# Kernel optimization log

Hardware: AMD Instinct MI355X
Metric: run time of the kernel (lower is better)

The kernel has to match this reference:

```python
import jax, jax.numpy as jnp
import numpy as np

NUM_GROUPS = 32
EPS = 1e-5


def group_norm(x, scale, bias):
    # x: [b, c, h, w]
    b, c, h, w = x.shape
    xg = x.reshape(b, NUM_GROUPS, c // NUM_GROUPS, h, w)
    mean = jnp.mean(xg, axis=(2, 3, 4), keepdims=True)
    var = jnp.var(xg, axis=(2, 3, 4), keepdims=True)
    xg = (xg - mean) * jax.lax.rsqrt(var + EPS)
    xn = xg.reshape(b, c, h, w)
    return xn * scale[None, :, None, None] + bias[None, :, None, None]


def conv1x1(x, w, b):
    # x: [b, c_in, h, w], w: [c_out, c_in], b: [c_out]
    return jnp.einsum('bchw,dc->bdhw', x, w) + b[None, :, None, None]


def setup_inputs() -> dict:
    key = jax.random.key(0)
    ks = jax.random.split(key, 11)
    B, C, H, W = 16, 512, 32, 32
    s = 1.0 / np.sqrt(C)
    inp = {
        'x': jax.random.normal(ks[0], (B, C, H, W), jnp.float32),
        'gn_scale': jnp.ones((C,), jnp.float32),
        'gn_bias': jnp.zeros((C,), jnp.float32),
        'wq': jax.random.normal(ks[1], (C, C), jnp.float32) * s,
        'bq': jnp.zeros((C,), jnp.float32),
        'wk': jax.random.normal(ks[2], (C, C), jnp.float32) * s,
        'bk': jnp.zeros((C,), jnp.float32),
        'wv': jax.random.normal(ks[3], (C, C), jnp.float32) * s,
        'bv': jnp.zeros((C,), jnp.float32),
        'wp': jax.random.normal(ks[4], (C, C), jnp.float32) * s,
        'bp': jnp.zeros((C,), jnp.float32),
    }
    return inp


def reference(x, gn_scale, gn_bias, wq, bq, wk, bk, wv, bv, wp, bp):
    b, c, h, w = x.shape
    xn = group_norm(x, gn_scale, gn_bias)
    q = conv1x1(xn, wq, bq).reshape(b, c, h * w)  # [b, c, n]
    k = conv1x1(xn, wk, bk).reshape(b, c, h * w)
    v = conv1x1(xn, wv, bv).reshape(b, c, h * w)
    # attn[b, i, j] = sum_c q[b, c, i] * k[b, c, j]
    attn = jnp.einsum('bci,bcj->bij', q, k) * (c ** -0.5)
    A = jax.nn.softmax(attn, axis=-1)
    # out[b, c, i] = sum_j A[b, i, j] * v[b, c, j]
    out = jnp.einsum('bij,bcj->bci', A, v).reshape(b, c, h, w)
    scores = conv1x1(out, wp, bp)
    return x + scores
```

## Files before the change

### kernel.cpp

```cpp
#include <hip/hip_runtime.h>

typedef __bf16 bf16x8 __attribute__((ext_vector_type(8)));
typedef float  f32x4  __attribute__((ext_vector_type(4)));

__device__ __forceinline__ unsigned short f2bf(float f) {
    union { float f; unsigned int u; } x; x.f = f;
    unsigned int r = (x.u + 0x7FFFu + ((x.u >> 16) & 1u)) >> 16;
    return (unsigned short)r;
}
__device__ __forceinline__ float bf2f(unsigned int hi) {
    union { unsigned int u; float f; } x; x.u = hi; return x.f;
}

typedef const __attribute__((address_space(1))) unsigned short gu16;
typedef __attribute__((address_space(3)))       unsigned short lu16;
__device__ __forceinline__ void gl_lds16(const unsigned short* g, unsigned short* l) {
    __builtin_amdgcn_global_load_lds((gu16*)g, (lu16*)l, 16, 0, 0);
}

__device__ __forceinline__ void gemm_core(
    const unsigned short* __restrict__ Ab, int lda,
    const unsigned short* __restrict__ Bb, int ldb,
    int K, f32x4 (&acc)[4][4],
    unsigned short* As, unsigned short* Bs)
{
    const int tid  = threadIdx.x;
    const int lane = tid & 63;
    const int wave = tid >> 6;
    const int wm   = (wave >> 1) * 64;
    const int wn   = (wave & 1) * 64;
    const int l16  = lane & 15;
    const int quad = lane >> 4;

    const int r0 = wave * 16 + (lane >> 2);
    const int c0 = (lane & 3) * 8;
    const unsigned short* gA0 = Ab + (long)r0 * lda + c0;
    const unsigned short* gA1 = gA0 + 64L * lda;
    const unsigned short* gB0 = Bb + (long)r0 * ldb + c0;
    const unsigned short* gB1 = gB0 + 64L * ldb;
    unsigned short* lA0 = As + wave * 512;
    unsigned short* lA1 = As + 2048 + wave * 512;
    unsigned short* lB0 = Bs + wave * 512;
    unsigned short* lB1 = Bs + 2048 + wave * 512;

    for (int k0 = 0; k0 < K; k0 += 64) {
        __syncthreads();
        gl_lds16(gA0 + k0, lA0);
        gl_lds16(gA1 + k0, lA1);
        gl_lds16(gB0 + k0, lB0);
        gl_lds16(gB1 + k0, lB1);
        gl_lds16(gA0 + k0 + 32, lA0 + 4096);
        gl_lds16(gA1 + k0 + 32, lA1 + 4096);
        gl_lds16(gB0 + k0 + 32, lB0 + 4096);
        gl_lds16(gB1 + k0 + 32, lB1 + 4096);
        __syncthreads();

        #pragma unroll
        for (int pan = 0; pan < 2; pan++) {
            const unsigned short* Ap = As + pan * 4096;
            const unsigned short* Bp = Bs + pan * 4096;
            bf16x8 af[4], bfr[4];
            #pragma unroll
            for (int mi = 0; mi < 4; mi++)
                af[mi] = *(const bf16x8*)&Ap[(wm + mi * 16 + l16) * 32 + quad * 8];
            #pragma unroll
            for (int ni = 0; ni < 4; ni++)
                bfr[ni] = *(const bf16x8*)&Bp[(wn + ni * 16 + l16) * 32 + quad * 8];
            #pragma unroll
            for (int mi = 0; mi < 4; mi++)
                #pragma unroll
                for (int ni = 0; ni < 4; ni++)
                    acc[mi][ni] = __builtin_amdgcn_mfma_f32_16x16x32_bf16(af[mi], bfr[ni], acc[mi][ni], 0, 0, 0);
        }
    }
}

template<typename OutT, bool TRANS_OUT, bool HAS_BIAS, bool HAS_RESID>
__global__ __launch_bounds__(256) void gemm_k(
    const unsigned short* __restrict__ Ag, long sA, int lda,
    const unsigned short* __restrict__ Bg, long sB, int ldb,
    OutT* __restrict__ Cg, long sC, int ldc,
    const float* __restrict__ bias,
    const float* __restrict__ resid, long sR,
    float alpha, int K)
{
    __shared__ __align__(16) unsigned short As[128 * 64];
    __shared__ __align__(16) unsigned short Bs[128 * 64];

    const unsigned short* Ab = Ag + (long)blockIdx.z * sA + (long)(blockIdx.y * 128) * lda;
    const unsigned short* Bb = Bg + (long)blockIdx.z * sB + (long)(blockIdx.x * 128) * ldb;

    f32x4 acc[4][4] = {};
    gemm_core(Ab, lda, Bb, ldb, K, acc, As, Bs);

    const int lane = threadIdx.x & 63;
    const int wave = threadIdx.x >> 6;
    const int l16  = lane & 15;
    const int quad = lane >> 4;
    const int mb = blockIdx.y * 128 + (wave >> 1) * 64;
    const int nb = blockIdx.x * 128 + (wave & 1) * 64;

    #pragma unroll
    for (int mi = 0; mi < 4; mi++) {
        #pragma unroll
        for (int ni = 0; ni < 4; ni++) {
            f32x4 v = acc[mi][ni];
            const int m0 = mb + mi * 16 + quad * 4;
            const int n  = nb + ni * 16 + l16;
            float o[4];
            #pragma unroll
            for (int r = 0; r < 4; r++) {
                float val = v[r] * alpha;
                if (HAS_BIAS) val += bias[m0 + r];
                o[r] = val;
            }
            if constexpr (!TRANS_OUT) {
                const long base = (long)blockIdx.z * sC;
                #pragma unroll
                for (int r = 0; r < 4; r++) {
                    float val = o[r];
                    if (HAS_RESID) val += resid[(long)blockIdx.z * sR + (long)(m0 + r) * ldc + n];
                    long idx = base + (long)(m0 + r) * ldc + n;
                    if constexpr (sizeof(OutT) == 2) ((unsigned short*)Cg)[idx] = f2bf(val);
                    else                              ((float*)Cg)[idx] = val;
                }
            } else {
                const long idx = (long)blockIdx.z * sC + (long)n * ldc + m0;
                if constexpr (sizeof(OutT) == 2) {
                    ushort4 p; p.x = f2bf(o[0]); p.y = f2bf(o[1]); p.z = f2bf(o[2]); p.w = f2bf(o[3]);
                    *(ushort4*)((unsigned short*)Cg + idx) = p;
                } else {
                    float4 p; p.x = o[0]; p.y = o[1]; p.z = o[2]; p.w = o[3];
                    *(float4*)((float*)Cg + idx) = p;
                }
            }
        }
    }
}

__global__ __launch_bounds__(256) void qkv_k(
    const unsigned short* __restrict__ Wqkv,
    const unsigned short* __restrict__ xnT,
    unsigned short* __restrict__ qT,
    unsigned short* __restrict__ kT,
    unsigned short* __restrict__ vB,
    const float* __restrict__ bqkv)
{
    __shared__ __align__(16) unsigned short As[128 * 64];
    __shared__ __align__(16) unsigned short Bs[128 * 64];

    const unsigned short* Ab = Wqkv + (long)(blockIdx.y * 128) * 512;
    const unsigned short* Bb = xnT + (long)blockIdx.z * 524288 + (long)(blockIdx.x * 128) * 512;

    f32x4 acc[4][4] = {};
    gemm_core(Ab, 512, Bb, 512, 512, acc, As, Bs);

    const int lane = threadIdx.x & 63;
    const int wave = threadIdx.x >> 6;
    const int l16  = lane & 15;
    const int quad = lane >> 4;
    const int mb = blockIdx.y * 128 + (wave >> 1) * 64;
    const int nb = blockIdx.x * 128 + (wave & 1) * 64;

    const int mat = blockIdx.y >> 2;
    const long zb = (long)blockIdx.z * 524288;

    #pragma unroll
    for (int mi = 0; mi < 4; mi++) {
        #pragma unroll
        for (int ni = 0; ni < 4; ni++) {
            f32x4 v = acc[mi][ni];
            const int m0 = mb + mi * 16 + quad * 4;
            const int n  = nb + ni * 16 + l16;
            float o[4];
            #pragma unroll
            for (int r = 0; r < 4; r++) o[r] = v[r] + bqkv[m0 + r];
            const int ml = m0 & 511;
            if (mat == 2) {
                #pragma unroll
                for (int r = 0; r < 4; r++)
                    vB[zb + (long)(ml + r) * 1024 + n] = f2bf(o[r]);
            } else {
                unsigned short* dst = (mat == 0) ? qT : kT;
                ushort4 p; p.x = f2bf(o[0]); p.y = f2bf(o[1]); p.z = f2bf(o[2]); p.w = f2bf(o[3]);
                *(ushort4*)(dst + zb + (long)n * 512 + ml) = p;
            }
        }
    }
}

__global__ __launch_bounds__(256) void softmax_k(unsigned short* __restrict__ S)
{
    const int wv   = threadIdx.x >> 6;
    const int lane = threadIdx.x & 63;
    const long row = (long)blockIdx.y * 1024 + blockIdx.x * 4 + wv;
    unsigned short* sp = S + row * 1024;

    uint4 u0 = ((const uint4*)sp)[lane];
    uint4 u1 = ((const uint4*)sp)[lane + 64];

    float f[16];
    const unsigned int* up = (const unsigned int*)&u0;
    #pragma unroll
    for (int i = 0; i < 4; i++) {
        f[2 * i]     = bf2f(up[i] << 16);
        f[2 * i + 1] = bf2f(up[i] & 0xFFFF0000u);
    }
    up = (const unsigned int*)&u1;
    #pragma unroll
    for (int i = 0; i < 4; i++) {
        f[8 + 2 * i] = bf2f(up[i] << 16);
        f[9 + 2 * i] = bf2f(up[i] & 0xFFFF0000u);
    }

    float mx = f[0];
    #pragma unroll
    for (int i = 1; i < 16; i++) mx = fmaxf(mx, f[i]);
    #pragma unroll
    for (int o = 1; o < 64; o <<= 1) mx = fmaxf(mx, __shfl_xor(mx, o));

    float sum = 0.f;
    #pragma unroll
    for (int i = 0; i < 16; i++) { f[i] = __expf(f[i] - mx); sum += f[i]; }
    #pragma unroll
    for (int o = 1; o < 64; o <<= 1) sum += __shfl_xor(sum, o);
    const float inv = 1.f / sum;

    uint4 w0, w1;
    unsigned int* wp = (unsigned int*)&w0;
    #pragma unroll
    for (int i = 0; i < 4; i++)
        wp[i] = (unsigned int)f2bf(f[2 * i] * inv) | ((unsigned int)f2bf(f[2 * i + 1] * inv) << 16);
    wp = (unsigned int*)&w1;
    #pragma unroll
    for (int i = 0; i < 4; i++)
        wp[i] = (unsigned int)f2bf(f[8 + 2 * i] * inv) | ((unsigned int)f2bf(f[9 + 2 * i] * inv) << 16);

    ((uint4*)sp)[lane]      = w0;
    ((uint4*)sp)[lane + 64] = w1;
}

__global__ __launch_bounds__(256) void gn_k(
    const float* __restrict__ x, const float* __restrict__ gsc,
    const float* __restrict__ gbi, unsigned short* __restrict__ xnT)
{
    __shared__ __align__(16) unsigned short ln[16 * 1024];
    __shared__ float red[8];
    const int b = blockIdx.y, g = blockIdx.x;
    const int tid = threadIdx.x, lane = tid & 63, wv = tid >> 6;

    const float4* x4 = (const float4*)(x + ((long)b * 512 + g * 16) * 1024);
    float4 vals[16];
    float s = 0.f, ss = 0.f;
    #pragma unroll
    for (int i = 0; i < 16; i++) {
        float4 v = x4[tid + i * 256];
        vals[i] = v;
        s  += v.x + v.y + v.z + v.w;
        ss += v.x * v.x + v.y * v.y + v.z * v.z + v.w * v.w;
    }
    for (int o = 32; o; o >>= 1) { s += __shfl_down(s, o); ss += __shfl_down(ss, o); }
    if (lane == 0) { red[wv * 2] = s; red[wv * 2 + 1] = ss; }
    __syncthreads();
    const float S  = red[0] + red[2] + red[4] + red[6];
    const float SS = red[1] + red[3] + red[5] + red[7];
    const float mean = S * (1.f / 16384.f);
    const float var  = SS * (1.f / 16384.f) - mean * mean;
    const float inv  = rsqrtf(var + 1e-5f);

    #pragma unroll
    for (int i = 0; i < 16; i++) {
        const int idx = tid + i * 256;
        const int c   = idx >> 8;
        const float sc = gsc[g * 16 + c] * inv;
        const float bi = gbi[g * 16 + c] - mean * sc;
        float4 v = vals[i];
        ushort4 p;
        p.x = f2bf(v.x * sc + bi); p.y = f2bf(v.y * sc + bi);
        p.z = f2bf(v.z * sc + bi); p.w = f2bf(v.w * sc + bi);
        ((ushort4*)ln)[idx] = p;
    }
    __syncthreads();

    unsigned short* op = xnT + (long)b * 1024 * 512 + g * 16;
    for (int rep = 0; rep < 4; rep++) {
        const int n = rep * 256 + tid;
        union { unsigned short u[16]; uint4 v[2]; } t;
        #pragma unroll
        for (int c = 0; c < 16; c++) t.u[c] = ln[c * 1024 + n];
        *(uint4*)&op[(long)n * 512]     = t.v[0];
        *(uint4*)&op[(long)n * 512 + 8] = t.v[1];
    }
}

__global__ __launch_bounds__(256) void wconv_k(
    const float* __restrict__ w0, const float* __restrict__ w1,
    const float* __restrict__ w2, const float* __restrict__ w3,
    const float* __restrict__ b0, const float* __restrict__ b1,
    const float* __restrict__ b2,
    unsigned short* __restrict__ out, float* __restrict__ bqkv)
{
    const int m = blockIdx.y;
    const int i = blockIdx.x * 256 + threadIdx.x;
    if (m == 4) {
        if (i < 384) {
            const int which = i >> 7, off = i & 127;
            const float* src = (which == 0) ? b0 : (which == 1) ? b1 : b2;
            ((float4*)bqkv)[i] = ((const float4*)src)[off];
        }
        return;
    }
    const float* src = (m == 0) ? w0 : (m == 1) ? w1 : (m == 2) ? w2 : w3;
    float4 v = ((const float4*)src)[i];
    ushort4 o; o.x = f2bf(v.x); o.y = f2bf(v.y); o.z = f2bf(v.z); o.w = f2bf(v.w);
    ((ushort4*)(out + (long)m * 262144))[i] = o;
}

extern "C" void kernel_launch(void* const* d_in, const int* in_sizes, int n_in,
                              void* d_out, int out_size, void* d_ws, size_t ws_size,
                              hipStream_t stream)
{
    const float* x   = (const float*)d_in[0];
    const float* gsc = (const float*)d_in[1];
    const float* gbi = (const float*)d_in[2];
    const float* wq  = (const float*)d_in[3];
    const float* bq  = (const float*)d_in[4];
    const float* wk  = (const float*)d_in[5];
    const float* bk  = (const float*)d_in[6];
    const float* wv  = (const float*)d_in[7];
    const float* bv  = (const float*)d_in[8];
    const float* wp  = (const float*)d_in[9];
    const float* bp  = (const float*)d_in[10];
    float* out = (float*)d_out;

    char* ws = (char*)d_ws;
    unsigned short* xnT = (unsigned short*)(ws);
    unsigned short* qT  = (unsigned short*)(ws + 16777216);
    unsigned short* kT  = (unsigned short*)(ws + 33554432);
    unsigned short* vB  = (unsigned short*)(ws + 50331648);
    unsigned short* Sb  = (unsigned short*)(ws + 67108864);
    unsigned short* Wb  = (unsigned short*)(ws + 100663296);
    float*          bqkv= (float*)        (ws + 102760448);
    unsigned short* OT  = xnT;

    const long sBCN = 512L * 1024;

    wconv_k<<<dim3(256, 5), 256, 0, stream>>>(wq, wk, wv, wp, bq, bk, bv, Wb, bqkv);
    gn_k<<<dim3(32, 16), 256, 0, stream>>>(x, gsc, gbi, xnT);

    qkv_k<<<dim3(8, 12, 16), 256, 0, stream>>>(Wb, xnT, qT, kT, vB, bqkv);

    gemm_k<unsigned short, false, false, false><<<dim3(8, 8, 16), 256, 0, stream>>>(
        qT, sBCN, 512, kT, sBCN, 512, Sb, 1048576L, 1024, nullptr, nullptr, 0,
        0.044194173824159216f, 512);
    softmax_k<<<dim3(256, 16), 256, 0, stream>>>(Sb);
    gemm_k<unsigned short, true, false, false><<<dim3(8, 4, 16), 256, 0, stream>>>(
        vB, sBCN, 1024, Sb, 1048576L, 1024, OT, sBCN, 512,
        nullptr, nullptr, 0, 1.f, 1024);
    gemm_k<float, false, true, true><<<dim3(8, 4, 16), 256, 0, stream>>>(
        Wb + 786432, 0, 512, OT, sBCN, 512, out, sBCN, 1024, bp, x, sBCN, 1.f, 512);
}
```

Baseline: 242.8 us.

## Template GEMM M-tile size, use 256x128 tiles for QKV and QK^T, shrink K step

```diff
diff --git a/kernel.cpp b/kernel.cpp
--- a/kernel.cpp
+++ b/kernel.cpp
@@ -18,65 +18,53 @@
     __builtin_amdgcn_global_load_lds((gu16*)g, (lu16*)l, 16, 0, 0);
 }
 
+template<int MF>
 __device__ __forceinline__ void gemm_core(
     const unsigned short* __restrict__ Ab, int lda,
     const unsigned short* __restrict__ Bb, int ldb,
-    int K, f32x4 (&acc)[4][4],
+    int K, f32x4 (&acc)[MF][4],
     unsigned short* As, unsigned short* Bs)
 {
     const int tid  = threadIdx.x;
     const int lane = tid & 63;
     const int wave = tid >> 6;
-    const int wm   = (wave >> 1) * 64;
+    const int wm   = (wave >> 1) * (MF * 16);
     const int wn   = (wave & 1) * 64;
     const int l16  = lane & 15;
     const int quad = lane >> 4;
 
     const int r0 = wave * 16 + (lane >> 2);
     const int c0 = (lane & 3) * 8;
-    const unsigned short* gA0 = Ab + (long)r0 * lda + c0;
-    const unsigned short* gA1 = gA0 + 64L * lda;
-    const unsigned short* gB0 = Bb + (long)r0 * ldb + c0;
-    const unsigned short* gB1 = gB0 + 64L * ldb;
-    unsigned short* lA0 = As + wave * 512;
-    unsigned short* lA1 = As + 2048 + wave * 512;
-    unsigned short* lB0 = Bs + wave * 512;
-    unsigned short* lB1 = Bs + 2048 + wave * 512;
-
-    for (int k0 = 0; k0 < K; k0 += 64) {
+
+    for (int k0 = 0; k0 < K; k0 += 32) {
         __syncthreads();
-        gl_lds16(gA0 + k0, lA0);
-        gl_lds16(gA1 + k0, lA1);
-        gl_lds16(gB0 + k0, lB0);
-        gl_lds16(gB1 + k0, lB1);
-        gl_lds16(gA0 + k0 + 32, lA0 + 4096);
-        gl_lds16(gA1 + k0 + 32, lA1 + 4096);
-        gl_lds16(gB0 + k0 + 32, lB0 + 4096);
-        gl_lds16(gB1 + k0 + 32, lB1 + 4096);
+        #pragma unroll
+        for (int ch = 0; ch < MF / 2; ch++)
+            gl_lds16(Ab + (long)(r0 + ch * 64) * lda + c0 + k0,
+                     As + ch * 2048 + wave * 512);
+        #pragma unroll
+        for (int ch = 0; ch < 2; ch++)
+            gl_lds16(Bb + (long)(r0 + ch * 64) * ldb + c0 + k0,
+                     Bs + ch * 2048 + wave * 512);
         __syncthreads();
 
-        #pragma unroll
-        for (int pan = 0; pan < 2; pan++) {
-            const unsigned short* Ap = As + pan * 4096;
-            const unsigned short* Bp = Bs + pan * 4096;
-            bf16x8 af[4], bfr[4];
-            #pragma unroll
-            for (int mi = 0; mi < 4; mi++)
-                af[mi] = *(const bf16x8*)&Ap[(wm + mi * 16 + l16) * 32 + quad * 8];
+        bf16x8 af[MF], bfr[4];
+        #pragma unroll
+        for (int mi = 0; mi < MF; mi++)
+            af[mi] = *(const bf16x8*)&As[(wm + mi * 16 + l16) * 32 + quad * 8];
+        #pragma unroll
+        for (int ni = 0; ni < 4; ni++)
+            bfr[ni] = *(const bf16x8*)&Bs[(wn + ni * 16 + l16) * 32 + quad * 8];
+        #pragma unroll
+        for (int mi = 0; mi < MF; mi++)
             #pragma unroll
             for (int ni = 0; ni < 4; ni++)
-                bfr[ni] = *(const bf16x8*)&Bp[(wn + ni * 16 + l16) * 32 + quad * 8];
-            #pragma unroll
-            for (int mi = 0; mi < 4; mi++)
-                #pragma unroll
-                for (int ni = 0; ni < 4; ni++)
-                    acc[mi][ni] = __builtin_amdgcn_mfma_f32_16x16x32_bf16(af[mi], bfr[ni], acc[mi][ni], 0, 0, 0);
-        }
-    }
-}
-
-template<typename OutT, bool TRANS_OUT, bool HAS_BIAS, bool HAS_RESID>
-__global__ __launch_bounds__(256) void gemm_k(
+                acc[mi][ni] = __builtin_amdgcn_mfma_f32_16x16x32_bf16(af[mi], bfr[ni], acc[mi][ni], 0, 0, 0);
+    }
+}
+
+template<int MF, typename OutT, bool TRANS_OUT, bool HAS_BIAS, bool HAS_RESID>
+__global__ __launch_bounds__(256, 2) void gemm_k(
     const unsigned short* __restrict__ Ag, long sA, int lda,
     const unsigned short* __restrict__ Bg, long sB, int ldb,
     OutT* __restrict__ Cg, long sC, int ldc,
@@ -84,24 +72,24 @@
     const float* __restrict__ resid, long sR,
     float alpha, int K)
 {
-    __shared__ __align__(16) unsigned short As[128 * 64];
-    __shared__ __align__(16) unsigned short Bs[128 * 64];
-
-    const unsigned short* Ab = Ag + (long)blockIdx.z * sA + (long)(blockIdx.y * 128) * lda;
+    __shared__ __align__(16) unsigned short As[MF * 1024];
+    __shared__ __align__(16) unsigned short Bs[128 * 32];
+
+    const unsigned short* Ab = Ag + (long)blockIdx.z * sA + (long)(blockIdx.y * MF * 32) * lda;
     const unsigned short* Bb = Bg + (long)blockIdx.z * sB + (long)(blockIdx.x * 128) * ldb;
 
-    f32x4 acc[4][4] = {};
-    gemm_core(Ab, lda, Bb, ldb, K, acc, As, Bs);
+    f32x4 acc[MF][4] = {};
+    gemm_core<MF>(Ab, lda, Bb, ldb, K, acc, As, Bs);
 
     const int lane = threadIdx.x & 63;
     const int wave = threadIdx.x >> 6;
     const int l16  = lane & 15;
     const int quad = lane >> 4;
-    const int mb = blockIdx.y * 128 + (wave >> 1) * 64;
+    const int mb = blockIdx.y * MF * 32 + (wave >> 1) * MF * 16;
     const int nb = blockIdx.x * 128 + (wave & 1) * 64;
 
     #pragma unroll
-    for (int mi = 0; mi < 4; mi++) {
+    for (int mi = 0; mi < MF; mi++) {
         #pragma unroll
         for (int ni = 0; ni < 4; ni++) {
             f32x4 v = acc[mi][ni];
@@ -138,7 +126,7 @@
     }
 }
 
-__global__ __launch_bounds__(256) void qkv_k(
+__global__ __launch_bounds__(256, 2) void qkv_k(
     const unsigned short* __restrict__ Wqkv,
     const unsigned short* __restrict__ xnT,
     unsigned short* __restrict__ qT,
@@ -146,27 +134,28 @@
     unsigned short* __restrict__ vB,
     const float* __restrict__ bqkv)
 {
-    __shared__ __align__(16) unsigned short As[128 * 64];
-    __shared__ __align__(16) unsigned short Bs[128 * 64];
-
-    const unsigned short* Ab = Wqkv + (long)(blockIdx.y * 128) * 512;
+    constexpr int MF = 8;
+    __shared__ __align__(16) unsigned short As[MF * 1024];
+    __shared__ __align__(16) unsigned short Bs[128 * 32];
+
+    const unsigned short* Ab = Wqkv + (long)(blockIdx.y * 256) * 512;
     const unsigned short* Bb = xnT + (long)blockIdx.z * 524288 + (long)(blockIdx.x * 128) * 512;
 
-    f32x4 acc[4][4] = {};
-    gemm_core(Ab, 512, Bb, 512, 512, acc, As, Bs);
+    f32x4 acc[MF][4] = {};
+    gemm_core<MF>(Ab, 512, Bb, 512, 512, acc, As, Bs);
 
     const int lane = threadIdx.x & 63;
     const int wave = threadIdx.x >> 6;
     const int l16  = lane & 15;
     const int quad = lane >> 4;
-    const int mb = blockIdx.y * 128 + (wave >> 1) * 64;
+    const int mb = blockIdx.y * 256 + (wave >> 1) * 128;
     const int nb = blockIdx.x * 128 + (wave & 1) * 64;
 
-    const int mat = blockIdx.y >> 2;
+    const int mat = blockIdx.y >> 1;
     const long zb = (long)blockIdx.z * 524288;
 
     #pragma unroll
-    for (int mi = 0; mi < 4; mi++) {
+    for (int mi = 0; mi < MF; mi++) {
         #pragma unroll
         for (int ni = 0; ni < 4; ni++) {
             f32x4 v = acc[mi][ni];
@@ -348,15 +337,15 @@
     wconv_k<<<dim3(256, 5), 256, 0, stream>>>(wq, wk, wv, wp, bq, bk, bv, Wb, bqkv);
     gn_k<<<dim3(32, 16), 256, 0, stream>>>(x, gsc, gbi, xnT);
 
-    qkv_k<<<dim3(8, 12, 16), 256, 0, stream>>>(Wb, xnT, qT, kT, vB, bqkv);
-
-    gemm_k<unsigned short, false, false, false><<<dim3(8, 8, 16), 256, 0, stream>>>(
+    qkv_k<<<dim3(8, 6, 16), 256, 0, stream>>>(Wb, xnT, qT, kT, vB, bqkv);
+
+    gemm_k<8, unsigned short, false, false, false><<<dim3(8, 4, 16), 256, 0, stream>>>(
         qT, sBCN, 512, kT, sBCN, 512, Sb, 1048576L, 1024, nullptr, nullptr, 0,
         0.044194173824159216f, 512);
     softmax_k<<<dim3(256, 16), 256, 0, stream>>>(Sb);
-    gemm_k<unsigned short, true, false, false><<<dim3(8, 4, 16), 256, 0, stream>>>(
+    gemm_k<4, unsigned short, true, false, false><<<dim3(8, 4, 16), 256, 0, stream>>>(
         vB, sBCN, 1024, Sb, 1048576L, 1024, OT, sBCN, 512,
         nullptr, nullptr, 0, 1.f, 1024);
-    gemm_k<float, false, true, true><<<dim3(8, 4, 16), 256, 0, stream>>>(
+    gemm_k<4, float, false, true, true><<<dim3(8, 4, 16), 256, 0, stream>>>(
         Wb + 786432, 0, 512, OT, sBCN, 512, out, sBCN, 1024, bp, x, sBCN, 1.f, 512);
 }
```

After: 250.2 us. +3.0%, slower.
